# Kernel optimization log

Hardware: AMD Instinct MI355X
Metric: run time of the kernel (lower is better)

Reference implementation:

```python
import jax, jax.numpy as jnp
import numpy as np

B, L, D = 2, 2048, 1024
H, K = 16, 16
HD = D // H


def setup_inputs() -> dict:
    key = jax.random.key(0)
    k1, k2, k3, k4, k5 = jax.random.split(key, 5)
    x = jax.random.normal(k1, (B, L, D), dtype=jnp.float32)
    # Linear weight (out_features, in_features), small init to keep logits sane
    w_in = jax.random.normal(k2, (3 * D, D), dtype=jnp.float32) * 0.02
    # TISA radial-basis kernel parameters, per (head, kernel)
    kernel_offsets = jax.random.normal(k3, (H, K), dtype=jnp.float32) * 20.0
    kernel_amplitudes = 0.1 + 0.01 * jax.random.normal(k4, (H, K), dtype=jnp.float32)
    kernel_sharpness = 0.1 + 0.01 * jax.random.normal(k5, (H, K), dtype=jnp.float32)
    return {"x": x, "w_in": w_in, "kernel_offsets": kernel_offsets,
            "kernel_amplitudes": kernel_amplitudes, "kernel_sharpness": kernel_sharpness}


def tisa_bias(offsets, amplitudes, sharpness, seq_len):
    # relative positions -(L-1) .. (L-1)  -> per-head RBF positional scores
    rel = jnp.arange(-(seq_len - 1), seq_len, dtype=jnp.float32)  # (2L-1,)
    # scores[h, m] = sum_k amp[h,k] * exp(-|sharp[h,k]| * (off[h,k] - rel[m])^2)
    diff = offsets[:, :, None] - rel[None, None, :]               # (H, K, 2L-1)
    scores = jnp.sum(amplitudes[:, :, None] * jnp.exp(-jnp.abs(sharpness)[:, :, None] * diff * diff), axis=1)  # (H, 2L-1)
    # Toeplitz expansion: bias[h, i, j] = scores[h, (i - j) + (L-1)]
    i = jnp.arange(seq_len)
    idx = i[:, None] - i[None, :] + (seq_len - 1)                 # (L, L)
    return scores[:, idx]                                         # (H, L, L)


def reference(x, w_in, kernel_offsets, kernel_amplitudes, kernel_sharpness):
    b, l, d = x.shape
    proj = jnp.einsum('bld,ed->ble', x, w_in)                     # (B, L, 3D)
    # split: memory = first 2D (k then v), query = last D
    k_, v_, q_ = proj[..., :d], proj[..., d:2 * d], proj[..., 2 * d:]

    def heads(t):
        return t.reshape(b, l, H, HD).transpose(0, 2, 1, 3)       # (B, H, L, HD)

    q, k, v = heads(q_), heads(k_), heads(v_)
    bias = tisa_bias(kernel_offsets, kernel_amplitudes, kernel_sharpness, l)  # (H, L, L)
    scale = 1.0 / np.sqrt(HD).astype(np.float32)
    logits = jnp.einsum('bhld,bhmd->bhlm', q, k) * scale + bias[None]
    attn = jax.nn.softmax(logits, axis=-1)
    out = jnp.einsum('bhlm,bhmd->bhld', attn, v)                  # (B, H, L, HD)
    return out.transpose(0, 2, 1, 3).reshape(b, l, d)             # (B, L, D)
```

## Files before the change

### kernel.cpp

```cpp
#include <hip/hip_runtime.h>
#include <hip/hip_bf16.h>
#include <stdint.h>
#include <stddef.h>


#define NB     2
#define NH     16
#define SL     2048
#define DH     64
#define DMODEL 1024
#define SCP    4096

typedef __attribute__((ext_vector_type(8))) short bf16x8;
typedef __attribute__((ext_vector_type(4))) short bf16x4;
typedef __attribute__((ext_vector_type(4))) float f32x4;

static __device__ __forceinline__ short f2bf(float x) {
  __hip_bfloat16 h = __float2bfloat16(x);
  return *reinterpret_cast<short*>(&h);
}
#define GLD(g, l) __builtin_amdgcn_global_load_lds( \
    (const __attribute__((address_space(1))) void*)(g), \
    (__attribute__((address_space(3))) void*)(l), 16, 0, 0)

__global__ __launch_bounds__(256) void cvt_bf16_k(const float* __restrict__ src,
                                                  short* __restrict__ dst, int n4) {
  int i = blockIdx.x * 256 + threadIdx.x;
  if (i >= n4) return;
  float4 a = *(const float4*)(src + (size_t)i * 4);
  bf16x4 o;
  o.x = f2bf(a.x); o.y = f2bf(a.y); o.z = f2bf(a.z); o.w = f2bf(a.w);
  *(bf16x4*)(dst + (size_t)i * 4) = o;
}

__global__ void tisa_bias_k(const float* __restrict__ koff,
                            const float* __restrict__ kamp,
                            const float* __restrict__ kshp,
                            float* __restrict__ scores) {
  int h = blockIdx.y;
  int r = blockIdx.x * 256 + threadIdx.x;
  if (r >= 4095) return;
  float rel = (float)(r - (SL - 1));
  float acc = 0.f;
#pragma unroll
  for (int k = 0; k < 16; ++k) {
    float o = koff[h * 16 + k];
    float a = kamp[h * 16 + k];
    float s = fabsf(kshp[h * 16 + k]);
    float d = o - rel;
    acc += a * __expf(-s * d * d);
  }
  scores[h * SCP + r] = acc;
}

__global__ __launch_bounds__(256) void qkv_gemm_k(
    const short* __restrict__ A, const short* __restrict__ Bw,
    __hip_bfloat16* __restrict__ kbuf, __hip_bfloat16* __restrict__ vbufT,
    __hip_bfloat16* __restrict__ qbuf) {
  __shared__ __align__(16) short As[128 * 64];
  __shared__ __align__(16) short Bs[128 * 64];
  const int tid  = threadIdx.x;
  const int lane = tid & 63;
  const int wv   = tid >> 6;
  const int l15  = lane & 15, quad = lane >> 4;
  const int wm = (wv & 1) * 64, wn = (wv >> 1) * 64;
  const int m0 = blockIdx.y * 128, n0 = blockIdx.x * 128;

  f32x4 acc[4][4];
#pragma unroll
  for (int r = 0; r < 4; ++r)
#pragma unroll
    for (int c = 0; c < 4; ++c) acc[r][c] = (f32x4){0.f, 0.f, 0.f, 0.f};

  for (int kt = 0; kt < 16; ++kt) {
    const int k0 = kt * 64;
#pragma unroll
    for (int it = 0; it < 4; ++it) {
      const int e8  = it * 256 + tid;
      const int row = e8 >> 3;
      const int col = (e8 & 7) * 8;
      GLD(A + (size_t)(m0 + row) * DMODEL + k0 + col, &As[e8 * 8]);
      GLD(Bw + (size_t)(n0 + row) * DMODEL + k0 + col, &Bs[e8 * 8]);
    }
    __syncthreads();
#pragma unroll
    for (int ki = 0; ki < 64; ki += 32) {
      bf16x8 af[4], bfv[4];
#pragma unroll
      for (int r = 0; r < 4; ++r)
        af[r] = *(const bf16x8*)&As[(wm + r * 16 + l15) * 64 + ki + quad * 8];
#pragma unroll
      for (int c = 0; c < 4; ++c)
        bfv[c] = *(const bf16x8*)&Bs[(wn + c * 16 + l15) * 64 + ki + quad * 8];
#pragma unroll
      for (int r = 0; r < 4; ++r)
#pragma unroll
        for (int c = 0; c < 4; ++c)
          acc[r][c] = __builtin_amdgcn_mfma_f32_16x16x32_bf16(af[r], bfv[c], acc[r][c], 0, 0, 0);
    }
    __syncthreads();
  }
#pragma unroll
  for (int c = 0; c < 4; ++c) {
    const int n     = n0 + wn + c * 16 + l15;
    const int which = n >> 10;
    const int hh    = (n >> 6) & 15;
    const int hd    = n & 63;
#pragma unroll
    for (int r = 0; r < 4; ++r) {
      const int m0r = m0 + wm + r * 16 + quad * 4;
      const int bb  = m0r >> 11;
      const int ll  = m0r & 2047;
      if (which == 1) {
        bf16x4 pk;
#pragma unroll
        for (int g = 0; g < 4; ++g) pk[g] = f2bf(acc[r][c][g]);
        *(bf16x4*)&vbufT[(((size_t)bb * NH + hh) * DH + hd) * SL + ll] = pk;
      } else if (which == 0) {
#pragma unroll
        for (int g = 0; g < 4; ++g)
          kbuf[(((size_t)bb * NH + hh) * SL + ll + g) * DH + hd] = __float2bfloat16(acc[r][c][g]);
      } else {
#pragma unroll
        for (int g = 0; g < 4; ++g)
          qbuf[(((size_t)bb * NH + hh) * SL + ll + g) * DH + hd] = __float2bfloat16(acc[r][c][g] * 0.125f);
      }
    }
  }
}

__global__ __launch_bounds__(256, 4) void attn_k(
    const __hip_bfloat16* __restrict__ qbuf, const __hip_bfloat16* __restrict__ kbuf,
    const __hip_bfloat16* __restrict__ vbufT, const float* __restrict__ scores,
    float* __restrict__ out) {
  __shared__ __align__(16) short Ks[64 * 72];
  __shared__ __align__(16) short Vs[64 * 72];
  __shared__ __align__(16) float Bss[2112];
  const int bh   = blockIdx.x;
  const int b    = bh >> 4, h = bh & 15;
  const int tid  = threadIdx.x;
  const int lane = tid & 63;
  const int wv   = tid >> 6;
  const int l15  = lane & 15, quad = lane >> 4;
  const int i0b  = blockIdx.y * 64;
  const int i0   = i0b + wv * 16;
  const __hip_bfloat16* qb = qbuf + (size_t)bh * SL * DH;
  const short* kb = (const short*)(kbuf + (size_t)bh * SL * DH);
  const short* vb = (const short*)(vbufT + (size_t)bh * DH * SL);
  const float* sc = scores + h * SCP;

  {
    const float* bsrc = sc + i0b;
    GLD(bsrc + (size_t)tid * 4, &Bss[tid * 4]);
    GLD(bsrc + (size_t)(256 + tid) * 4, &Bss[(256 + tid) * 4]);
    if (tid < 16) GLD(bsrc + (size_t)(512 + tid) * 4, &Bss[(512 + tid) * 4]);
  }

  bf16x8 qf0 = *(const bf16x8*)&qb[(size_t)(i0 + l15) * DH + quad * 8];
  bf16x8 qf1 = *(const bf16x8*)&qb[(size_t)(i0 + l15) * DH + 32 + quad * 8];

  f32x4 o[4];
#pragma unroll
  for (int d = 0; d < 4; ++d) o[d] = (f32x4){0.f, 0.f, 0.f, 0.f};
  float lsum = 0.f;

  for (int j0 = 0; j0 < SL; j0 += 64) {
    {
      const short* ksrc = kb + (size_t)j0 * DH;
      int c0 = tid;          int r0 = c0 / 9, s0 = c0 - r0 * 9;
      GLD(ksrc + (size_t)r0 * DH + s0 * 8, &Ks[c0 * 8]);
      int c1 = 256 + tid;    int r1 = c1 / 9, s1 = c1 - r1 * 9;
      GLD(ksrc + (size_t)r1 * DH + s1 * 8, &Ks[c1 * 8]);
      if (tid < 64) {
        int c2 = 512 + tid;  int r2 = c2 / 9, s2 = c2 - r2 * 9;
        GLD(ksrc + (size_t)r2 * DH + s2 * 8, &Ks[c2 * 8]);
      }
    }
    {
      int c0 = tid;          int r0 = c0 / 9, s0 = c0 - r0 * 9;
      GLD(vb + (size_t)r0 * SL + j0 + s0 * 8, &Vs[c0 * 8]);
      int c1 = 256 + tid;    int r1 = c1 / 9, s1 = c1 - r1 * 9;
      GLD(vb + (size_t)r1 * SL + j0 + s1 * 8, &Vs[c1 * 8]);
      if (tid < 64) {
        int c2 = 512 + tid;  int r2 = c2 / 9, s2 = c2 - r2 * 9;
        GLD(vb + (size_t)r2 * SL + j0 + s2 * 8, &Vs[c2 * 8]);
      }
    }
    __syncthreads();

    f32x4 s[4];
#pragma unroll
    for (int sub = 0; sub < 4; ++sub) {
      const short* kr = &Ks[(sub * 16 + l15) * 72];
      bf16x8 a0 = *(const bf16x8*)&kr[quad * 8];
      bf16x8 a1 = *(const bf16x8*)&kr[32 + quad * 8];
      f32x4 z = (f32x4){0.f, 0.f, 0.f, 0.f};
      z      = __builtin_amdgcn_mfma_f32_16x16x32_bf16(a0, qf0, z, 0, 0, 0);
      s[sub] = __builtin_amdgcn_mfma_f32_16x16x32_bf16(a1, qf1, z, 0, 0, 0);
    }
    bf16x4 pf[4];
    const int bb0 = wv * 16 + l15 - j0 + 2047 - quad * 4;
#pragma unroll
    for (int sub = 0; sub < 4; ++sub) {
      const int ib = bb0 - sub * 16;
#pragma unroll
      for (int r = 0; r < 4; ++r) {
        const float p = __expf(s[sub][r] + Bss[ib - r]);
        lsum += p;
        pf[sub][r] = f2bf(p);
      }
    }
#pragma unroll
    for (int d = 0; d < 4; ++d) {
      const short* vr = &Vs[(d * 16 + l15) * 72];
#pragma unroll
      for (int sub = 0; sub < 4; ++sub) {
        bf16x4 vfrag = *(const bf16x4*)&vr[sub * 16 + quad * 4];
        o[d] = __builtin_amdgcn_mfma_f32_16x16x16bf16_1k(vfrag, pf[sub], o[d], 0, 0, 0);
      }
    }
    __syncthreads();
  }

  lsum += __shfl_xor(lsum, 16);
  lsum += __shfl_xor(lsum, 32);
  const float inv = 1.f / lsum;
  float* orow = out + (((size_t)b * SL + i0 + l15) * NH + h) * DH;
#pragma unroll
  for (int d = 0; d < 4; ++d) {
    f32x4 v;
#pragma unroll
    for (int g = 0; g < 4; ++g) v[g] = o[d][g] * inv;
    *(f32x4*)&orow[d * 16 + quad * 4] = v;
  }
}

extern "C" void kernel_launch(void* const* d_in, const int* in_sizes, int n_in,
                              void* d_out, int out_size, void* d_ws, size_t ws_size,
                              hipStream_t stream) {
  const float* x    = (const float*)d_in[0];
  const float* w    = (const float*)d_in[1];
  const float* koff = (const float*)d_in[2];
  const float* kamp = (const float*)d_in[3];
  const float* kshp = (const float*)d_in[4];
  float* out = (float*)d_out;

  const size_t per = (size_t)NB * NH * SL * DH;
  const size_t nx  = (size_t)NB * SL * DMODEL;
  const size_t nw  = (size_t)3 * DMODEL * DMODEL;

  __hip_bfloat16* kbuf  = (__hip_bfloat16*)d_ws;
  __hip_bfloat16* vbufT = kbuf + per;
  __hip_bfloat16* qbuf  = vbufT + per;
  float* scores = (float*)(qbuf + per);
  short* xbf    = (short*)(scores + (size_t)NH * SCP);
  short* wbf    = xbf + nx;

  cvt_bf16_k<<<(int)(nx / 4 + 255) / 256, 256, 0, stream>>>(x, xbf, (int)(nx / 4));
  cvt_bf16_k<<<(int)(nw / 4 + 255) / 256, 256, 0, stream>>>(w, wbf, (int)(nw / 4));
  tisa_bias_k<<<dim3(16, NH), 256, 0, stream>>>(koff, kamp, kshp, scores);
  qkv_gemm_k<<<dim3(24, 32), 256, 0, stream>>>(xbf, wbf, kbuf, vbufT, qbuf);
  attn_k<<<dim3(NB * NH, SL / 64), 256, 0, stream>>>(qbuf, kbuf, vbufT, scores, out);
}
```

Measured before the change: 202.7 us.

## Switch attention kernel to 32x32x16 MFMA tiles with two waves per block

Rewrites the attention kernel so each wave handles 32 query rows using 32x32x16 bf16 MFMA for both QK^T and PV, instead of 16-row tiles with 16x16 MFMAs. The block shrinks to 128 threads (2 waves) covering the same 64 rows, and P fragments are exchanged across half-waves with shuffles to form the B operand. Larger MFMA tiles raise math per LDS read and cut instruction count. The cost is fewer waves per block, more accumulator registers, and lower latency hiding and occupancy.

```diff
diff --git a/kernel.cpp b/kernel.cpp
--- a/kernel.cpp
+++ b/kernel.cpp
@@ -11,13 +11,20 @@
 #define DMODEL 1024
 #define SCP    4096
 
-typedef __attribute__((ext_vector_type(8))) short bf16x8;
-typedef __attribute__((ext_vector_type(4))) short bf16x4;
-typedef __attribute__((ext_vector_type(4))) float f32x4;
+typedef __attribute__((ext_vector_type(8)))  short bf16x8;
+typedef __attribute__((ext_vector_type(4)))  short bf16x4;
+typedef __attribute__((ext_vector_type(4)))  float f32x4;
+typedef __attribute__((ext_vector_type(16))) float f32x16;
 
 static __device__ __forceinline__ short f2bf(float x) {
   __hip_bfloat16 h = __float2bfloat16(x);
   return *reinterpret_cast<short*>(&h);
+}
+static __device__ __forceinline__ long long bf4_to_ll(bf16x4 v) {
+  long long r; __builtin_memcpy(&r, &v, 8); return r;
+}
+static __device__ __forceinline__ bf16x4 ll_to_bf4(long long v) {
+  bf16x4 r; __builtin_memcpy(&r, &v, 8); return r;
 }
 #define GLD(g, l) __builtin_amdgcn_global_load_lds( \
     (const __attribute__((address_space(1))) void*)(g), \
@@ -129,7 +136,7 @@
   }
 }
 
-__global__ __launch_bounds__(256, 4) void attn_k(
+__global__ __launch_bounds__(128, 2) void attn_k(
     const __hip_bfloat16* __restrict__ qbuf, const __hip_bfloat16* __restrict__ kbuf,
     const __hip_bfloat16* __restrict__ vbufT, const float* __restrict__ scores,
     float* __restrict__ out) {
@@ -141,9 +148,9 @@
   const int tid  = threadIdx.x;
   const int lane = tid & 63;
   const int wv   = tid >> 6;
-  const int l15  = lane & 15, quad = lane >> 4;
+  const int n32  = lane & 31, hf = lane >> 5;
   const int i0b  = blockIdx.y * 64;
-  const int i0   = i0b + wv * 16;
+  const int i0   = i0b + wv * 32;
   const __hip_bfloat16* qb = qbuf + (size_t)bh * SL * DH;
   const short* kb = (const short*)(kbuf + (size_t)bh * SL * DH);
   const short* vb = (const short*)(vbufT + (size_t)bh * DH * SL);
@@ -151,88 +158,104 @@
 
   {
     const float* bsrc = sc + i0b;
-    GLD(bsrc + (size_t)tid * 4, &Bss[tid * 4]);
-    GLD(bsrc + (size_t)(256 + tid) * 4, &Bss[(256 + tid) * 4]);
+#pragma unroll
+    for (int i = 0; i < 4; ++i)
+      GLD(bsrc + (size_t)(i * 128 + tid) * 4, &Bss[(i * 128 + tid) * 4]);
     if (tid < 16) GLD(bsrc + (size_t)(512 + tid) * 4, &Bss[(512 + tid) * 4]);
   }
 
-  bf16x8 qf0 = *(const bf16x8*)&qb[(size_t)(i0 + l15) * DH + quad * 8];
-  bf16x8 qf1 = *(const bf16x8*)&qb[(size_t)(i0 + l15) * DH + 32 + quad * 8];
-
-  f32x4 o[4];
-#pragma unroll
-  for (int d = 0; d < 4; ++d) o[d] = (f32x4){0.f, 0.f, 0.f, 0.f};
+  bf16x8 qf[4];
+#pragma unroll
+  for (int kc = 0; kc < 4; ++kc)
+    qf[kc] = *(const bf16x8*)&qb[(size_t)(i0 + n32) * DH + kc * 16 + hf * 8];
+
+  f32x16 ot[2];
+#pragma unroll
+  for (int dt = 0; dt < 2; ++dt)
+#pragma unroll
+    for (int r = 0; r < 16; ++r) ot[dt][r] = 0.f;
   float lsum = 0.f;
 
   for (int j0 = 0; j0 < SL; j0 += 64) {
     {
       const short* ksrc = kb + (size_t)j0 * DH;
-      int c0 = tid;          int r0 = c0 / 9, s0 = c0 - r0 * 9;
-      GLD(ksrc + (size_t)r0 * DH + s0 * 8, &Ks[c0 * 8]);
-      int c1 = 256 + tid;    int r1 = c1 / 9, s1 = c1 - r1 * 9;
-      GLD(ksrc + (size_t)r1 * DH + s1 * 8, &Ks[c1 * 8]);
+#pragma unroll
+      for (int i = 0; i < 4; ++i) {
+        int c = i * 128 + tid; int r = c / 9, s = c - r * 9;
+        GLD(ksrc + (size_t)r * DH + s * 8, &Ks[c * 8]);
+      }
       if (tid < 64) {
-        int c2 = 512 + tid;  int r2 = c2 / 9, s2 = c2 - r2 * 9;
-        GLD(ksrc + (size_t)r2 * DH + s2 * 8, &Ks[c2 * 8]);
+        int c = 512 + tid; int r = c / 9, s = c - r * 9;
+        GLD(ksrc + (size_t)r * DH + s * 8, &Ks[c * 8]);
       }
     }
     {
-      int c0 = tid;          int r0 = c0 / 9, s0 = c0 - r0 * 9;
-      GLD(vb + (size_t)r0 * SL + j0 + s0 * 8, &Vs[c0 * 8]);
-      int c1 = 256 + tid;    int r1 = c1 / 9, s1 = c1 - r1 * 9;
-      GLD(vb + (size_t)r1 * SL + j0 + s1 * 8, &Vs[c1 * 8]);
+#pragma unroll
+      for (int i = 0; i < 4; ++i) {
+        int c = i * 128 + tid; int r = c / 9, s = c - r * 9;
+        GLD(vb + (size_t)r * SL + j0 + s * 8, &Vs[c * 8]);
+      }
       if (tid < 64) {
-        int c2 = 512 + tid;  int r2 = c2 / 9, s2 = c2 - r2 * 9;
-        GLD(vb + (size_t)r2 * SL + j0 + s2 * 8, &Vs[c2 * 8]);
-      }
-    }
-    __syncthreads();
-
-    f32x4 s[4];
-#pragma unroll
-    for (int sub = 0; sub < 4; ++sub) {
-      const short* kr = &Ks[(sub * 16 + l15) * 72];
-      bf16x8 a0 = *(const bf16x8*)&kr[quad * 8];
-      bf16x8 a1 = *(const bf16x8*)&kr[32 + quad * 8];
-      f32x4 z = (f32x4){0.f, 0.f, 0.f, 0.f};
-      z      = __builtin_amdgcn_mfma_f32_16x16x32_bf16(a0, qf0, z, 0, 0, 0);
-      s[sub] = __builtin_amdgcn_mfma_f32_16x16x32_bf16(a1, qf1, z, 0, 0, 0);
-    }
-    bf16x4 pf[4];
-    const int bb0 = wv * 16 + l15 - j0 + 2047 - quad * 4;
-#pragma unroll
-    for (int sub = 0; sub < 4; ++sub) {
-      const int ib = bb0 - sub * 16;
-#pragma unroll
-      for (int r = 0; r < 4; ++r) {
-        const float p = __expf(s[sub][r] + Bss[ib - r]);
-        lsum += p;
-        pf[sub][r] = f2bf(p);
-      }
-    }
-#pragma unroll
-    for (int d = 0; d < 4; ++d) {
-      const short* vr = &Vs[(d * 16 + l15) * 72];
-#pragma unroll
-      for (int sub = 0; sub < 4; ++sub) {
-        bf16x4 vfrag = *(const bf16x4*)&vr[sub * 16 + quad * 4];
-        o[d] = __builtin_amdgcn_mfma_f32_16x16x16bf16_1k(vfrag, pf[sub], o[d], 0, 0, 0);
-      }
-    }
-    __syncthreads();
-  }
-
-  lsum += __shfl_xor(lsum, 16);
+        int c = 512 + tid; int r = c / 9, s = c - r * 9;
+        GLD(vb + (size_t)r * SL + j0 + s * 8, &Vs[c * 8]);
+      }
+    }
+    __syncthreads();
+
+#pragma unroll
+    for (int kt = 0; kt < 2; ++kt) {
+      f32x16 st;
+#pragma unroll
+      for (int r = 0; r < 16; ++r) st[r] = 0.f;
+#pragma unroll
+      for (int kc = 0; kc < 4; ++kc) {
+        bf16x8 kf = *(const bf16x8*)&Ks[(kt * 32 + n32) * 72 + kc * 16 + hf * 8];
+        st = __builtin_amdgcn_mfma_f32_32x32x16_bf16(kf, qf[kc], st, 0, 0, 0);
+      }
+      bf16x4 pk[4];
+      const int tb0 = wv * 32 + n32 - j0 - kt * 32 - 4 * hf + 2047;
+#pragma unroll
+      for (int g = 0; g < 4; ++g) {
+        const int tb = tb0 - 8 * g;
+#pragma unroll
+        for (int i = 0; i < 4; ++i) {
+          const float p = __expf(st[g * 4 + i] + Bss[tb - i]);
+          lsum += p;
+          pk[g][i] = f2bf(p);
+        }
+      }
+      long long s0 = hf ? bf4_to_ll(pk[0]) : bf4_to_ll(pk[1]);
+      bf16x4 r0 = ll_to_bf4(__shfl_xor(s0, 32));
+      bf16x8 pf0 = hf == 0 ? __builtin_shufflevector(pk[0], r0, 0, 1, 2, 3, 4, 5, 6, 7)
+                           : __builtin_shufflevector(r0, pk[1], 0, 1, 2, 3, 4, 5, 6, 7);
+      long long s1 = hf ? bf4_to_ll(pk[2]) : bf4_to_ll(pk[3]);
+      bf16x4 r1 = ll_to_bf4(__shfl_xor(s1, 32));
+      bf16x8 pf1 = hf == 0 ? __builtin_shufflevector(pk[2], r1, 0, 1, 2, 3, 4, 5, 6, 7)
+                           : __builtin_shufflevector(r1, pk[3], 0, 1, 2, 3, 4, 5, 6, 7);
+#pragma unroll
+      for (int dt = 0; dt < 2; ++dt) {
+        const short* vr = &Vs[(dt * 32 + n32) * 72 + kt * 32];
+        bf16x8 vf0 = *(const bf16x8*)&vr[hf * 8];
+        bf16x8 vf1 = *(const bf16x8*)&vr[16 + hf * 8];
+        ot[dt] = __builtin_amdgcn_mfma_f32_32x32x16_bf16(vf0, pf0, ot[dt], 0, 0, 0);
+        ot[dt] = __builtin_amdgcn_mfma_f32_32x32x16_bf16(vf1, pf1, ot[dt], 0, 0, 0);
+      }
+    }
+    __syncthreads();
+  }
+
   lsum += __shfl_xor(lsum, 32);
   const float inv = 1.f / lsum;
-  float* orow = out + (((size_t)b * SL + i0 + l15) * NH + h) * DH;
-#pragma unroll
-  for (int d = 0; d < 4; ++d) {
-    f32x4 v;
-#pragma unroll
-    for (int g = 0; g < 4; ++g) v[g] = o[d][g] * inv;
-    *(f32x4*)&orow[d * 16 + quad * 4] = v;
-  }
+  float* orow = out + (((size_t)b * SL + i0 + n32) * NH + h) * DH;
+#pragma unroll
+  for (int dt = 0; dt < 2; ++dt)
+#pragma unroll
+    for (int g = 0; g < 4; ++g) {
+      f32x4 v;
+#pragma unroll
+      for (int i = 0; i < 4; ++i) v[i] = ot[dt][g * 4 + i] * inv;
+      *(f32x4*)&orow[dt * 32 + 8 * g + 4 * hf] = v;
+    }
 }
 
 extern "C" void kernel_launch(void* const* d_in, const int* in_sizes, int n_in,
@@ -260,5 +283,5 @@
   cvt_bf16_k<<<(int)(nw / 4 + 255) / 256, 256, 0, stream>>>(w, wbf, (int)(nw / 4));
   tisa_bias_k<<<dim3(16, NH), 256, 0, stream>>>(koff, kamp, kshp, scores);
   qkv_gemm_k<<<dim3(24, 32), 256, 0, stream>>>(xbf, wbf, kbuf, vbufT, qbuf);
-  attn_k<<<dim3(NB * NH, SL / 64), 256, 0, stream>>>(qbuf, kbuf, vbufT, scores, out);
-}
+  attn_k<<<dim3(NB * NH, SL / 64), 128, 0, stream>>>(qbuf, kbuf, vbufT, scores, out);
+}
```

New measurement: 202.6 us. Within noise of the previous version (-0.0%).
